# Optimization experiments

Measured on AMD Instinct MI355X. Metric: run time of the kernel, lower is better.

The kernel has to match this reference:

```python
import jax, jax.numpy as jnp
import numpy as np

B, S, T, D, H, FF = 2, 512, 64, 256, 8, 1024
DK = D // H
EPS = 1e-5


def setup_inputs() -> dict:
    key = jax.random.key(0)
    ks = jax.random.split(key, 24)
    sc = 1.0 / np.sqrt(D)
    inp = {"x": jax.random.normal(ks[0], (B, S, T, D), jnp.float32)}
    names = ["tq", "tk", "tv", "to", "sq", "sk", "sv", "so"]
    for i, n in enumerate(names):
        inp[n + "_w"] = jax.random.normal(ks[1 + 2 * i], (D, D), jnp.float32) * sc
        inp[n + "_b"] = jax.random.normal(ks[2 + 2 * i], (D,), jnp.float32) * sc
    inp["fc1_w"] = jax.random.normal(ks[17], (D, FF), jnp.float32) * sc
    inp["fc1_b"] = jnp.zeros((FF,), jnp.float32)
    inp["fc2_w"] = jax.random.normal(ks[18], (FF, D), jnp.float32) * (1.0 / np.sqrt(FF))
    inp["fc2_b"] = jnp.zeros((D,), jnp.float32)
    inp["ln1_w"] = jnp.ones((D,), jnp.float32)
    inp["ln1_b"] = jnp.zeros((D,), jnp.float32)
    inp["ln2_w"] = jnp.ones((D,), jnp.float32)
    inp["ln2_b"] = jnp.zeros((D,), jnp.float32)
    return inp


def _heads(x, w, b):
    # (B,S,T,D) -> (B,H,S,T,DK)
    Bx, Sx, Tx, Dx = x.shape
    return (x @ w + b).reshape(Bx, Sx, Tx, H, Dx // H).transpose(0, 3, 1, 2, 4)


def _merge(o, w, b):
    # (B,H,S,T,DK) -> (B,S,T,D)
    Bx, Hx, Sx, Tx, dk = o.shape
    return o.transpose(0, 2, 3, 1, 4).reshape(Bx, Sx, Tx, Hx * dk) @ w + b


def _ln(x, g, b):
    m = jnp.mean(x, -1, keepdims=True)
    v = jnp.mean((x - m) ** 2, -1, keepdims=True)
    return (x - m) * jax.lax.rsqrt(v + EPS) * g + b


def _forward(x, tq_w, tq_b, tk_w, tk_b, tv_w, tv_b, to_w, to_b,
             sq_w, sq_b, sk_w, sk_b, sv_w, sv_b, so_w, so_b,
             fc1_w, fc1_b, fc2_w, fc2_b, ln1_w, ln1_b, ln2_w, ln2_b):
    scale = 1.0 / np.sqrt(DK)
    # --- time attention (over T, independent per space point s) ---
    q = _heads(x, tq_w, tq_b)
    k = _heads(x, tk_w, tk_b)
    v = _heads(x, tv_w, tv_b)
    p = jax.nn.softmax(jnp.einsum('bhstd,bhsud->bhstu', q, k) * scale, axis=-1)
    tt = _merge(jnp.einsum('bhstu,bhsud->bhstd', p, v), to_w, to_b)
    # --- space attention (over S, independent per time step t) ---
    q = _heads(tt, sq_w, sq_b)
    k = _heads(tt, sk_w, sk_b)
    v = _heads(tt, sv_w, sv_b)
    p = jax.nn.softmax(jnp.einsum('bhstd,bhutd->bhtsu', q, k) * scale, axis=-1)
    so = _merge(jnp.einsum('bhtsu,bhutd->bhstd', p, v), so_w, so_b)
    # --- residual + post-LN, then FFN + residual + post-LN ---
    h = _ln(x + so, ln1_w, ln1_b)
    ff = jax.nn.relu(h @ fc1_w + fc1_b) @ fc2_w + fc2_b
    return _ln(h + ff, ln2_w, ln2_b)


def reference(x, tq_w, tq_b, tk_w, tk_b, tv_w, tv_b, to_w, to_b,
              sq_w, sq_b, sk_w, sk_b, sv_w, sv_b, so_w, so_b,
              fc1_w, fc1_b, fc2_w, fc2_b, ln1_w, ln1_b, ln2_w, ln2_b):
    return _forward(x, tq_w, tq_b, tk_w, tk_b, tv_w, tv_b, to_w, to_b,
                    sq_w, sq_b, sk_w, sk_b, sv_w, sv_b, so_w, so_b,
                    fc1_w, fc1_b, fc2_w, fc2_b, ln1_w, ln1_b, ln2_w, ln2_b)
```

## Files before the change

### kernel.cpp

```cpp
#include <hip/hip_runtime.h>
#include <hip/hip_bf16.h>

#define BB   2
#define SS   512
#define TT_  64
#define DD   256
#define HH   8
#define DKK  32
#define FFF  1024
#define NTOK 65536
#define EPSV 1e-5f
#define SCALE 0.17677669529663687f
#define S2F   0.25503486f
#define KPS  40
#define KP   40
#define VH   136
#define VP6  80

typedef unsigned short u16;
typedef unsigned int   u32;
typedef __attribute__((ext_vector_type(8))) short bf16x8;
typedef __attribute__((ext_vector_type(4))) short bf16x4;
typedef __attribute__((ext_vector_type(4))) float f32x4;

#if __has_builtin(__builtin_amdgcn_exp2f)
#define EXP2(x) __builtin_amdgcn_exp2f(x)
#else
#define EXP2(x) exp2f(x)
#endif

__device__ __forceinline__ float bf2f(u32 u) {
    union { u32 i; float f; } c; c.i = u << 16; return c.f;
}
__device__ __forceinline__ u16 f2bf(float f) {
    __hip_bfloat16 h = __float2bfloat16(f);
    return *reinterpret_cast<u16*>(&h);
}
__device__ __forceinline__ u32 cvtpk2(float lo, float hi) {
    float2 f; f.x = lo; f.y = hi;
    __hip_bfloat162 h2 = __float22bfloat162_rn(f);
    union { __hip_bfloat162 h; u32 u; } c; c.h = h2;
    return c.u;
}
__device__ __forceinline__ void load8v(const float* p, float* v) {
    *(float4*)(v)     = *(const float4*)(p);
    *(float4*)(v + 4) = *(const float4*)(p + 4);
}
__device__ __forceinline__ void load8v(const u16* p, float* v) {
    uint4 raw = *(const uint4*)(p);
    v[0] = bf2f(raw.x & 0xffffu); v[1] = bf2f(raw.x >> 16);
    v[2] = bf2f(raw.y & 0xffffu); v[3] = bf2f(raw.y >> 16);
    v[4] = bf2f(raw.z & 0xffffu); v[5] = bf2f(raw.z >> 16);
    v[6] = bf2f(raw.w & 0xffffu); v[7] = bf2f(raw.w >> 16);
}
__device__ __forceinline__ void load4v(const float* p, float* v) {
    float4 t = *(const float4*)p; v[0] = t.x; v[1] = t.y; v[2] = t.z; v[3] = t.w;
}
__device__ __forceinline__ void load4v(const u16* p, float* v) {
    uint2 raw = *(const uint2*)p;
    v[0] = bf2f(raw.x & 0xffffu); v[1] = bf2f(raw.x >> 16);
    v[2] = bf2f(raw.y & 0xffffu); v[3] = bf2f(raw.y >> 16);
}
__device__ __forceinline__ uint4 pack8bf(const float* v) {
    uint4 r;
    r.x = cvtpk2(v[0], v[1]); r.y = cvtpk2(v[2], v[3]);
    r.z = cvtpk2(v[4], v[5]); r.w = cvtpk2(v[6], v[7]);
    return r;
}
__device__ __forceinline__ uint2 pack4bf(const float* v) {
    uint2 r;
    r.x = cvtpk2(v[0], v[1]); r.y = cvtpk2(v[2], v[3]);
    return r;
}
__device__ __forceinline__ bf16x4 packbf4(const float* v) {
    union { uint2 u; bf16x4 h; } c;
    c.u = pack4bf(v);
    return c.h;
}
__device__ __forceinline__ void store4o(float* p, const float* v) {
    float4 t; t.x = v[0]; t.y = v[1]; t.z = v[2]; t.w = v[3];
    *(float4*)p = t;
}
__device__ __forceinline__ void store4o(u16* p, const float* v) {
    *(uint2*)p = pack4bf(v);
}
__device__ __forceinline__ void gl16(const u16* gsrc, u16* ldst) {
    __builtin_amdgcn_global_load_lds(
        (const __attribute__((address_space(1))) void*)gsrc,
        (__attribute__((address_space(3))) void*)ldst, 16, 0, 0);
}

#if __has_builtin(__builtin_amdgcn_mfma_f32_16x16x16bf16_1k)
__device__ __forceinline__ f32x4 mfma16(bf16x4 a, bf16x4 b, f32x4 c) {
    return __builtin_amdgcn_mfma_f32_16x16x16bf16_1k(a, b, c, 0, 0, 0);
}
#else
__device__ __forceinline__ f32x4 mfma16(bf16x4 a, bf16x4 b, f32x4 c) {
    asm("v_mfma_f32_16x16x16_bf16 %0, %1, %2, %0" : "+v"(c) : "v"(a), "v"(b));
    return c;
}
#endif

#define BF16_ONE ((short)0x3F80)

__global__ __launch_bounds__(256)
void transpose_w(const float* __restrict__ W, u16* __restrict__ WT, int K, int M,
                 float scale)
{
    __shared__ float t[32][33];
    const int mb = blockIdx.x * 32;
    const int kb = blockIdx.y * 32;
    const int lx = threadIdx.x & 31;
    const int ly = threadIdx.x >> 5;
    #pragma unroll
    for (int i = ly; i < 32; i += 8) t[i][lx] = W[(size_t)(kb + i) * M + mb + lx];
    __syncthreads();
    #pragma unroll
    for (int i = ly; i < 32; i += 8) WT[(size_t)(mb + i) * K + kb + lx] = f2bf(t[lx][i] * scale);
}

__global__ __launch_bounds__(256)
void pack_bias3(const float* __restrict__ a, const float* __restrict__ b,
                const float* __restrict__ c, float* __restrict__ out, float s0)
{
    const int i = threadIdx.x;
    out[i] = a[i] * s0; out[256 + i] = b[i]; out[512 + i] = c[i];
}

__global__ __launch_bounds__(256)
void fuse_to_sqkv_w(const float* __restrict__ to_w,
                    const float* __restrict__ sq_w, const float* __restrict__ sk_w,
                    const float* __restrict__ sv_w, u16* __restrict__ wt_out)
{
    const int m = blockIdx.x;
    const int k = threadIdx.x;
    const float* Wsq = (m < 256) ? sq_w : (m < 512 ? sk_w : sv_w);
    const int mc = m & 255;
    float acc = 0.f;
    for (int j = 0; j < 256; j++)
        acc += to_w[k * 256 + j] * Wsq[j * 256 + mc];
    if (m < 256) acc *= S2F;
    wt_out[m * 256 + k] = f2bf(acc);
}
__global__ __launch_bounds__(256)
void fuse_to_sqkv_b(const float* __restrict__ to_b,
                    const float* __restrict__ sq_w, const float* __restrict__ sk_w,
                    const float* __restrict__ sv_w,
                    const float* __restrict__ sq_b, const float* __restrict__ sk_b,
                    const float* __restrict__ sv_b, float* __restrict__ b_out)
{
    const int m = blockIdx.x * 256 + threadIdx.x;
    const float* Wsq = (blockIdx.x == 0) ? sq_w : (blockIdx.x == 1 ? sk_w : sv_w);
    const float* bs  = (blockIdx.x == 0) ? sq_b : (blockIdx.x == 1 ? sk_b : sv_b);
    const int mc = m & 255;
    float acc = bs[mc];
    for (int j = 0; j < 256; j++) acc += to_b[j] * Wsq[j * 256 + mc];
    if (blockIdx.x == 0) acc *= S2F;
    b_out[m] = acc;
}

__global__ __launch_bounds__(256)
void cvt_bf16(const float* __restrict__ in, u16* __restrict__ out, int n8)
{
    for (int i = blockIdx.x * blockDim.x + threadIdx.x; i < n8; i += gridDim.x * blockDim.x) {
        float v[8];
        load8v(in + (size_t)i * 8, v);
        *(uint4*)(out + (size_t)i * 8) = pack8bf(v);
    }
}

__global__ __launch_bounds__(512)
void gemm_bt6(const u16* __restrict__ A, int lda,
              const u16* __restrict__ WT,
              const float* __restrict__ bias, u16* __restrict__ C,
              int K, int M, int relu)
{
    __shared__ u16 As0[256 * 32];
    __shared__ u16 As1[256 * 32];
    __shared__ u16 Bs0[128 * 32];
    __shared__ u16 Bs1[128 * 32];
    const int tid  = threadIdx.x;
    const int wid  = tid >> 6;
    const int lane = tid & 63;
    const int l16  = lane & 15;
    const int kg   = lane >> 4;

    const int nwg = gridDim.x * gridDim.y;
    int lin = blockIdx.y * gridDim.x + blockIdx.x;
    lin = (lin & 7) * (nwg >> 3) + (lin >> 3);
    const int row0 = (lin / gridDim.x) * 256;
    const int col0 = (lin % gridDim.x) * 128;

    const int srow = lane >> 2;
    const int gchunk = ((lane & 3) ^ ((srow >> 1) & 3)) * 8;
    const int rchunk = (kg ^ ((l16 >> 1) & 3)) * 8;

    const u16* Abase = A  + (size_t)(row0 + srow) * lda + gchunk;
    const u16* Bbase = WT + (size_t)(col0 + wid * 16 + srow) * K + gchunk;

    f32x4 acc[2][8];
    #pragma unroll
    for (int fr = 0; fr < 2; fr++)
        #pragma unroll
        for (int fc = 0; fc < 8; fc++)
            acc[fr][fc] = (f32x4){0.f, 0.f, 0.f, 0.f};

#define STAGE_T(ASB, BSB, k0)                                                   \
    do {                                                                        \
        _Pragma("unroll")                                                       \
        for (int q = 0; q < 2; q++) {                                           \
            const int rbase = wid * 32 + q * 16;                                \
            gl16(Abase + (size_t)rbase * lda + (k0), &ASB[rbase * 32]);         \
        }                                                                       \
        gl16(Bbase + (k0), &BSB[wid * 16 * 32]);                                \
    } while (0)

#define COMPUTE_T(ASB, BSB)                                                     \
    do {                                                                        \
        bf16x8 af[2], bfr[8];                                                   \
        _Pragma("unroll")                                                       \
        for (int fr = 0; fr < 2; fr++)                                          \
            af[fr] = *(const bf16x8*)(&ASB[(wid * 32 + fr * 16 + l16) * 32 + rchunk]); \
        _Pragma("unroll")                                                       \
        for (int fc = 0; fc < 8; fc++)                                          \
            bfr[fc] = *(const bf16x8*)(&BSB[(fc * 16 + l16) * 32 + rchunk]);    \
        _Pragma("unroll")                                                       \
        for (int fr = 0; fr < 2; fr++)                                          \
            _Pragma("unroll")                                                   \
            for (int fc = 0; fc < 8; fc++)                                      \
                acc[fr][fc] = __builtin_amdgcn_mfma_f32_16x16x32_bf16(af[fr], bfr[fc], acc[fr][fc], 0, 0, 0); \
    } while (0)

    STAGE_T(As0, Bs0, 0);
    __syncthreads();

    for (int k0 = 0; k0 < K; k0 += 64) {
        if (k0 + 32 < K) STAGE_T(As1, Bs1, k0 + 32);
        COMPUTE_T(As0, Bs0);
        __syncthreads();
        if (k0 + 64 < K) STAGE_T(As0, Bs0, k0 + 64);
        COMPUTE_T(As1, Bs1);
        __syncthreads();
    }
#undef STAGE_T
#undef COMPUTE_T

    #pragma unroll
    for (int fr = 0; fr < 2; fr++) {
        #pragma unroll
        for (int fc = 0; fc < 8; fc++) {
            const int col = col0 + fc * 16 + l16;
            const float bv = bias[col];
            const int row = row0 + wid * 32 + fr * 16 + kg * 4;
            #pragma unroll
            for (int j = 0; j < 4; j += 2) {
                float x0 = acc[fr][fc][j]     + bv;
                float x1 = acc[fr][fc][j + 1] + bv;
                if (relu) { x0 = fmaxf(x0, 0.f); x1 = fmaxf(x1, 0.f); }
                const u32 pk = cvtpk2(x0, x1);
                C[(size_t)(row + j)     * M + col] = (u16)pk;
                C[(size_t)(row + j + 1) * M + col] = (u16)(pk >> 16);
            }
        }
    }
}

__global__ __launch_bounds__(512)
void gemm_bt6h(const u16* __restrict__ A, int lda,
               const u16* __restrict__ WT,
               const float* __restrict__ bias, u16* __restrict__ C,
               int K, int M, int relu)
{
    __shared__ u16 As0[128 * 32];
    __shared__ u16 As1[128 * 32];
    __shared__ u16 Bs0[128 * 32];
    __shared__ u16 Bs1[128 * 32];
    const int tid  = threadIdx.x;
    const int wid  = tid >> 6;
    const int lane = tid & 63;
    const int l16  = lane & 15;
    const int kg   = lane >> 4;

    const int nwg = gridDim.x * gridDim.y;
    int lin = blockIdx.y * gridDim.x + blockIdx.x;
    lin = (lin & 7) * (nwg >> 3) + (lin >> 3);
    const int row0 = (lin / gridDim.x) * 128;
    const int col0 = (lin % gridDim.x) * 128;

    const int srow = lane >> 2;
    const int gchunk = ((lane & 3) ^ ((srow >> 1) & 3)) * 8;
    const int rchunk = (kg ^ ((l16 >> 1) & 3)) * 8;

    const u16* Abase = A  + (size_t)(row0 + wid * 16 + srow) * lda + gchunk;
    const u16* Bbase = WT + (size_t)(col0 + wid * 16 + srow) * K + gchunk;

    f32x4 acc[8];
    #pragma unroll
    for (int fc = 0; fc < 8; fc++)
        acc[fc] = (f32x4){0.f, 0.f, 0.f, 0.f};

#define STAGE_H(ASB, BSB, k0)                                                   \
    do {                                                                        \
        gl16(Abase + (k0), &ASB[wid * 16 * 32]);                                \
        gl16(Bbase + (k0), &BSB[wid * 16 * 32]);                                \
    } while (0)

#define COMPUTE_H(ASB, BSB)                                                     \
    do {                                                                        \
        bf16x8 af, bfr[8];                                                      \
        af = *(const bf16x8*)(&ASB[(wid * 16 + l16) * 32 + rchunk]);            \
        _Pragma("unroll")                                                       \
        for (int fc = 0; fc < 8; fc++)                                          \
            bfr[fc] = *(const bf16x8*)(&BSB[(fc * 16 + l16) * 32 + rchunk]);    \
        _Pragma("unroll")                                                       \
        for (int fc = 0; fc < 8; fc++)                                          \
            acc[fc] = __builtin_amdgcn_mfma_f32_16x16x32_bf16(af, bfr[fc], acc[fc], 0, 0, 0); \
    } while (0)

    STAGE_H(As0, Bs0, 0);
    __syncthreads();

    for (int k0 = 0; k0 < K; k0 += 64) {
        if (k0 + 32 < K) STAGE_H(As1, Bs1, k0 + 32);
        COMPUTE_H(As0, Bs0);
        __syncthreads();
        if (k0 + 64 < K) STAGE_H(As0, Bs0, k0 + 64);
        COMPUTE_H(As1, Bs1);
        __syncthreads();
    }
#undef STAGE_H
#undef COMPUTE_H

    #pragma unroll
    for (int fc = 0; fc < 8; fc++) {
        const int col = col0 + fc * 16 + l16;
        const float bv = bias[col];
        const int row = row0 + wid * 16 + kg * 4;
        #pragma unroll
        for (int j = 0; j < 4; j += 2) {
            float x0 = acc[fc][j]     + bv;
            float x1 = acc[fc][j + 1] + bv;
            if (relu) { x0 = fmaxf(x0, 0.f); x1 = fmaxf(x1, 0.f); }
            const u32 pk = cvtpk2(x0, x1);
            C[(size_t)(row + j)     * M + col] = (u16)pk;
            C[(size_t)(row + j + 1) * M + col] = (u16)(pk >> 16);
        }
    }
}

__global__ __launch_bounds__(256)
void time_attn12(const u16* __restrict__ F, int ld, u16* __restrict__ O)
{
    __shared__ u16 Ks2[2][64 * KP];
    __shared__ u16 Vt2[2][32 * VP6];
    const int bid = blockIdx.x;
    const int tid  = threadIdx.x;
    const int wid  = tid >> 6;
    const int lane = tid & 63;
    const int l16  = lane & 15;
    const int g    = lane >> 4;

    #pragma unroll
    for (int it = 0; it < 2; it++) {
        const int i = tid + it * 256;
        const int tu = i >> 8, rr = (i >> 2) & 63, p = i & 3;
        const int tau = bid * 2 + tu;
        const size_t ga = ((size_t)(tau >> 3) * 64 + rr) * ld + (tau & 7) * DKK + 256 + p * 8;
        *(uint4*)&Ks2[tu][rr * KP + p * 8] = *(const uint4*)(F + ga);
    }
    #pragma unroll
    for (int it = 0; it < 2; it++) {
        const int i = tid + it * 256;
        const int tu = i >> 8, p = (i >> 6) & 3, rr = i & 63;
        const int tau = bid * 2 + tu;
        const size_t ga = ((size_t)(tau >> 3) * 64 + rr) * ld + (tau & 7) * DKK + 512 + p * 8;
        uint4 vv = *(const uint4*)(F + ga);
        const u16* vp = (const u16*)&vv;
        #pragma unroll
        for (int j = 0; j < 8; j++) Vt2[tu][(p * 8 + j) * VP6 + rr] = vp[j];
    }
    __syncthreads();

    const int tu  = wid >> 1;
    const int tau = bid * 2 + tu;
    const int hc  = (tau & 7) * DKK;
    const size_t n0 = (size_t)(tau >> 3) * 64;
    const int q0  = (wid & 1) * 32;
    const f32x4 z4 = (f32x4){0.f, 0.f, 0.f, 0.f};
    const bf16x4 vone = (bf16x4){BF16_ONE, BF16_ONE, BF16_ONE, BF16_ONE};

    bf16x8 qf[2];
    #pragma unroll
    for (int f = 0; f < 2; f++)
        qf[f] = *(const bf16x8*)(F + (n0 + q0 + f * 16 + l16) * ld + hc + g * 8);

    f32x4 s[2][4];
    #pragma unroll
    for (int kt = 0; kt < 4; kt++) {
        bf16x8 kf = *(const bf16x8*)&Ks2[tu][(kt * 16 + l16) * KP + g * 8];
        s[0][kt] = __builtin_amdgcn_mfma_f32_16x16x32_bf16(kf, qf[0], z4, 0, 0, 0);
        s[1][kt] = __builtin_amdgcn_mfma_f32_16x16x32_bf16(kf, qf[1], z4, 0, 0, 0);
    }

    bf16x4 pp[2][4];
    #pragma unroll
    for (int f = 0; f < 2; f++) {
        #pragma unroll
        for (int kt = 0; kt < 4; kt++) {
            float pv[4];
            #pragma unroll
            for (int j = 0; j < 4; j++) pv[j] = EXP2(s[f][kt][j]);
            pp[f][kt] = packbf4(pv);
        }
    }

    f32x4 o[2][2];
    f32x4 lacc[2];
    #pragma unroll
    for (int f = 0; f < 2; f++) {
        lacc[f] = z4;
        #pragma unroll
        for (int hh = 0; hh < 2; hh++)
            o[f][hh] = z4;
    }
    #pragma unroll
    for (int kt = 0; kt < 4; kt++) {
        bf16x4 vf[2];
        #pragma unroll
        for (int hh = 0; hh < 2; hh++)
            vf[hh] = *(const bf16x4*)&Vt2[tu][(hh * 16 + l16) * VP6 + kt * 16 + g * 4];
        #pragma unroll
        for (int f = 0; f < 2; f++) {
            o[f][0] = mfma16(pp[f][kt], vf[0], o[f][0]);
            o[f][1] = mfma16(pp[f][kt], vf[1], o[f][1]);
            lacc[f] = mfma16(pp[f][kt], vone, lacc[f]);
        }
    }

    #pragma unroll
    for (int f = 0; f < 2; f++) {
        float iv[4];
        #pragma unroll
        for (int j = 0; j < 4; j++) iv[j] = 1.f / lacc[f][j];
        #pragma unroll
        for (int hh = 0; hh < 2; hh++) {
            const u32 p0 = cvtpk2(o[f][hh][0] * iv[0], o[f][hh][1] * iv[1]);
            const u32 p1 = cvtpk2(o[f][hh][2] * iv[2], o[f][hh][3] * iv[3]);
            const size_t ga0 = (n0 + q0 + f * 16 + g * 4) * DD + hc + hh * 16 + l16;
            O[ga0]          = (u16)p0;
            O[ga0 + DD]     = (u16)(p0 >> 16);
            O[ga0 + 2 * DD] = (u16)p1;
            O[ga0 + 3 * DD] = (u16)(p1 >> 16);
        }
    }
}

__global__ __launch_bounds__(512, 4)
void space_attn16(u16* __restrict__ F, int ld)
{
    __shared__ u16 Ks[2][128 * KPS];
    __shared__ u16 Vt[2][32 * VH];
    const int bid = blockIdx.x;
    const int t  = bid & (TT_ - 1);
    const int h  = (bid >> 6) & (HH - 1);
    const int b  = bid >> 9;
    const int hc = h * DKK;
    const int tid  = threadIdx.x;
    const int wid  = tid >> 6;
    const int lane = tid & 63;
    const int l16  = lane & 15;
    const int g    = lane >> 4;

    const int kr = tid >> 2, kp = tid & 3;
    const int vr = tid & 127, vp = tid >> 7;
    const size_t rowstr = (size_t)TT_ * ld;
    const size_t base0  = ((size_t)(b * SS) * TT_ + t) * ld + hc;

    const int q0 = wid * 64;
    bf16x8 qf[4];
    #pragma unroll
    for (int f = 0; f < 4; f++) {
        const int s = q0 + f * 16 + l16;
        qf[f] = *(const bf16x8*)(F + base0 + (size_t)s * rowstr + g * 8);
    }

    uint4 kreg = *(const uint4*)(F + base0 + 256 + (size_t)kr * rowstr + kp * 8);
    uint4 vreg = *(const uint4*)(F + base0 + 512 + (size_t)vr * rowstr + vp * 8);
    *(uint4*)&Ks[0][kr * KPS + kp * 8] = kreg;
    {
        const u16* vpp = (const u16*)&vreg;
        #pragma unroll
        for (int j = 0; j < 8; j++) Vt[0][(vp * 8 + j) * VH + vr] = vpp[j];
    }
    __syncthreads();

    f32x4 o[4][2];
    f32x4 lacc[4];
    const f32x4 z4 = (f32x4){0.f, 0.f, 0.f, 0.f};
    const bf16x4 vone = (bf16x4){BF16_ONE, BF16_ONE, BF16_ONE, BF16_ONE};
    #pragma unroll
    for (int f = 0; f < 4; f++) {
        lacc[f] = z4;
        #pragma unroll
        for (int hh = 0; hh < 2; hh++)
            o[f][hh] = z4;
    }

    for (int qtr = 0; qtr < 4; qtr++) {
        const int cur = qtr & 1;
        if (qtr < 3) {
            const int key = (qtr + 1) * 128;
            kreg = *(const uint4*)(F + base0 + 256 + (size_t)(key + kr) * rowstr + kp * 8);
            vreg = *(const uint4*)(F + base0 + 512 + (size_t)(key + vr) * rowstr + vp * 8);
        }

        for (int kc2 = 0; kc2 < 4; kc2++) {
            bf16x8 kfa = *(const bf16x8*)&Ks[cur][(kc2 * 32 +      l16) * KPS + g * 8];
            bf16x8 kfb = *(const bf16x8*)&Ks[cur][(kc2 * 32 + 16 + l16) * KPS + g * 8];

            bf16x4 pa[4], pb[4];
            #pragma unroll
            for (int f = 0; f < 4; f++) {
                f32x4 sa = __builtin_amdgcn_mfma_f32_16x16x32_bf16(kfa, qf[f], z4, 0, 0, 0);
                f32x4 sb = __builtin_amdgcn_mfma_f32_16x16x32_bf16(kfb, qf[f], z4, 0, 0, 0);
                float pva[4], pvb[4];
                #pragma unroll
                for (int j = 0; j < 4; j++) pva[j] = EXP2(sa[j]);
                #pragma unroll
                for (int j = 0; j < 4; j++) pvb[j] = EXP2(sb[j]);
                pa[f] = packbf4(pva);
                pb[f] = packbf4(pvb);
            }

            bf16x4 va[2][2];
            #pragma unroll
            for (int hh = 0; hh < 2; hh++)
                #pragma unroll
                for (int u = 0; u < 2; u++)
                    va[hh][u] = *(const bf16x4*)&Vt[cur][(hh * 16 + l16) * VH + kc2 * 32 + u * 16 + g * 4];

            __builtin_amdgcn_s_setprio(1);
            #pragma unroll
            for (int f = 0; f < 4; f++) {
                #pragma unroll
                for (int hh = 0; hh < 2; hh++) {
                    o[f][hh] = mfma16(pa[f], va[hh][0], o[f][hh]);
                    o[f][hh] = mfma16(pb[f], va[hh][1], o[f][hh]);
                }
                lacc[f] = mfma16(pa[f], vone, lacc[f]);
                lacc[f] = mfma16(pb[f], vone, lacc[f]);
            }
            __builtin_amdgcn_s_setprio(0);
        }

        if (qtr < 3) {
            __syncthreads();
            *(uint4*)&Ks[cur ^ 1][kr * KPS + kp * 8] = kreg;
            const u16* vpp = (const u16*)&vreg;
            #pragma unroll
            for (int j = 0; j < 8; j++) Vt[cur ^ 1][(vp * 8 + j) * VH + vr] = vpp[j];
            __syncthreads();
        }
    }

    #pragma unroll
    for (int f = 0; f < 4; f++) {
        float iv[4];
        #pragma unroll
        for (int j = 0; j < 4; j++) iv[j] = 1.f / lacc[f][j];
        const int s = q0 + f * 16 + g * 4;
        #pragma unroll
        for (int hh = 0; hh < 2; hh++) {
            const u32 p0 = cvtpk2(o[f][hh][0] * iv[0], o[f][hh][1] * iv[1]);
            const u32 p1 = cvtpk2(o[f][hh][2] * iv[2], o[f][hh][3] * iv[3]);
            const size_t ga0 = base0 + (size_t)s * rowstr + hh * 16 + l16;
            F[ga0]              = (u16)p0;
            F[ga0 + rowstr]     = (u16)(p0 >> 16);
            F[ga0 + 2 * rowstr] = (u16)p1;
            F[ga0 + 3 * rowstr] = (u16)(p1 >> 16);
        }
    }
}

template<typename T1, typename TO>
__global__ __launch_bounds__(256)
void add_ln(const T1* __restrict__ X1, const u16* __restrict__ X2,
            const float* __restrict__ gw, const float* __restrict__ bw,
            TO* __restrict__ out)
{
    const int row  = blockIdx.x * 4 + (threadIdx.x >> 6);
    const int lane = threadIdx.x & 63;
    const size_t base = (size_t)row * DD + lane * 4;
    float v[4], w2[4];
    load4v(X1 + base, v);
    load4v(X2 + base, w2);
    v[0] += w2[0]; v[1] += w2[1]; v[2] += w2[2]; v[3] += w2[3];
    float s1 = v[0] + v[1] + v[2] + v[3];
    float s2 = v[0]*v[0] + v[1]*v[1] + v[2]*v[2] + v[3]*v[3];
    #pragma unroll
    for (int o = 1; o < 64; o <<= 1) { s1 += __shfl_xor(s1, o); s2 += __shfl_xor(s2, o); }
    const float mean = s1 * (1.f / DD);
    const float var  = s2 * (1.f / DD) - mean * mean;
    const float rs   = rsqrtf(var + EPSV);
    float o4[4];
    #pragma unroll
    for (int i = 0; i < 4; i++) {
        const int d = lane * 4 + i;
        o4[i] = (v[i] - mean) * rs * gw[d] + bw[d];
    }
    store4o(out + base, o4);
}

extern "C" void kernel_launch(void* const* d_in, const int* in_sizes, int n_in,
                              void* d_out, int out_size, void* d_ws, size_t ws_size,
                              hipStream_t stream)
{
    (void)in_sizes; (void)n_in; (void)out_size;
    const float* x     = (const float*)d_in[0];
    const float* tq_w  = (const float*)d_in[1];
    const float* tq_b  = (const float*)d_in[2];
    const float* tk_w  = (const float*)d_in[3];
    const float* tk_b  = (const float*)d_in[4];
    const float* tv_w  = (const float*)d_in[5];
    const float* tv_b  = (const float*)d_in[6];
    const float* to_w  = (const float*)d_in[7];
    const float* to_b  = (const float*)d_in[8];
    const float* sq_w  = (const float*)d_in[9];
    const float* sq_b  = (const float*)d_in[10];
    const float* sk_w  = (const float*)d_in[11];
    const float* sk_b  = (const float*)d_in[12];
    const float* sv_w  = (const float*)d_in[13];
    const float* sv_b  = (const float*)d_in[14];
    const float* so_w  = (const float*)d_in[15];
    const float* so_b  = (const float*)d_in[16];
    const float* fc1_w = (const float*)d_in[17];
    const float* fc1_b = (const float*)d_in[18];
    const float* fc2_w = (const float*)d_in[19];
    const float* fc2_b = (const float*)d_in[20];
    const float* ln1_w = (const float*)d_in[21];
    const float* ln1_b = (const float*)d_in[22];
    const float* ln2_w = (const float*)d_in[23];
    const float* ln2_b = (const float*)d_in[24];

    const size_t SLOT = (size_t)NTOK * DD;
    u16*   F  = (u16*)d_ws;
    u16*   W0 = (u16*)d_ws;
    u16*   W1 = W0 + SLOT;
    u16*   OA = (u16*)d_out;
    float* HD = (float*)d_out;
    u16*   WTb = (u16*)((char*)d_out + (61u << 20));
    float* BIb = (float*)((char*)d_out + (63u << 20));

    const bool ffn1 = ws_size >= 6 * SLOT * sizeof(u16);
    u16* W2 = ffn1 ? (W1 + 4 * SLOT) : (W1 + SLOT);

    u16* wt_tqkv  = WTb;
    u16* wt_fused = wt_tqkv + 3 * 65536;
    u16* wt_so    = wt_fused + 3 * 65536;
    u16* wt_fc1   = wt_so + 65536;
    u16* wt_fc2   = wt_fc1 + 262144;
    float* b_tqkv  = BIb;
    float* b_fused = BIb + 768;

    dim3 blk(256);
    dim3 blk5(512);
    dim3 gT(DD / 32, DD / 32);

    transpose_w<<<gT, blk, 0, stream>>>(tq_w, wt_tqkv,              DD, DD, S2F);
    transpose_w<<<gT, blk, 0, stream>>>(tk_w, wt_tqkv + 65536,      DD, DD, 1.0f);
    transpose_w<<<gT, blk, 0, stream>>>(tv_w, wt_tqkv + 2 * 65536,  DD, DD, 1.0f);
    transpose_w<<<gT, blk, 0, stream>>>(so_w, wt_so, DD, DD, 1.0f);
    transpose_w<<<dim3(FFF / 32, DD / 32), blk, 0, stream>>>(fc1_w, wt_fc1, DD, FFF, 1.0f);
    transpose_w<<<dim3(DD / 32, FFF / 32), blk, 0, stream>>>(fc2_w, wt_fc2, FFF, DD, 1.0f);
    pack_bias3<<<1, blk, 0, stream>>>(tq_b, tk_b, tv_b, b_tqkv, S2F);
    fuse_to_sqkv_w<<<768, blk, 0, stream>>>(to_w, sq_w, sk_w, sv_w, wt_fused);
    fuse_to_sqkv_b<<<3, blk, 0, stream>>>(to_b, sq_w, sk_w, sv_w, sq_b, sk_b, sv_b, b_fused);

    cvt_bf16<<<2048, blk, 0, stream>>>(x, OA, (int)(SLOT / 8));

    dim3 gqkv(768 / 128, NTOK / 256);
    dim3 gd(DD / 128, NTOK / 256);

    gemm_bt6<<<gqkv, blk5, 0, stream>>>(OA, DD, wt_tqkv, b_tqkv, F, DD, 768, 0);
    time_attn12<<<BB * HH * SS / 2, blk, 0, stream>>>(F, 768, OA);

    gemm_bt6<<<gqkv, blk5, 0, stream>>>(OA, DD, wt_fused, b_fused, F, DD, 768, 0);
    space_attn16<<<BB * HH * TT_, blk5, 0, stream>>>(F, 768);
    gemm_bt6<<<gd, blk5, 0, stream>>>(F, 768, wt_so, so_b, OA, DD, DD, 0);

    add_ln<float, u16><<<NTOK / 4, blk, 0, stream>>>(x, OA, ln1_w, ln1_b, W0);

    if (ffn1) {
        gemm_bt6<<<dim3(FFF / 128, NTOK / 256), blk5, 0, stream>>>(W0, DD, wt_fc1, fc1_b, W1, DD, FFF, 1);
        gemm_bt6h<<<dim3(DD / 128, NTOK / 128), blk5, 0, stream>>>(W1, FFF, wt_fc2, fc2_b, W2, FFF, DD, 0);
        add_ln<u16, float><<<NTOK / 4, blk, 0, stream>>>(W0, W2, ln2_w, ln2_b, HD);
    } else {
        for (int c = 0; c < 4; c++) {
            const size_t off = (size_t)c * 16384 * DD;
            gemm_bt6<<<dim3(FFF / 128, 16384 / 256), blk5, 0, stream>>>(W0 + off, DD, wt_fc1, fc1_b, W1, DD, FFF, 1);
            gemm_bt6h<<<dim3(DD / 128, 16384 / 128), blk5, 0, stream>>>(W1, FFF, wt_fc2, fc2_b, W2, FFF, DD, 0);
            add_ln<u16, float><<<16384 / 4, blk, 0, stream>>>(W0 + off, W2, ln2_w, ln2_b, HD + off);
        }
    }
}
```

Baseline: 420.0 us.

## Fuse LayerNorm epilogues into full-row output GEMMs for so-proj and fc2

Adds a gemm_ln kernel in which each workgroup computes a 128x256 tile covering the full D width. Bias, residual add and LayerNorm run in the epilogue using in-wave shuffles. This replaces the so-projection GEMM plus add_ln and the fc2 GEMM plus add_ln, which removes two intermediate activation round trips through memory and two launches. The trade-offs are fewer workgroups (512) with 16 accumulator tiles per wave, so register pressure rises and occupancy may drop. Workspace layout also changes: weights move into the workspace when it is large enough.

Result: faster. 406.3 us (-3.3%).

```diff
diff --git a/kernel.cpp b/kernel.cpp
--- a/kernel.cpp
+++ b/kernel.cpp
@@ -84,6 +84,10 @@
 __device__ __forceinline__ void store4o(u16* p, const float* v) {
     *(uint2*)p = pack4bf(v);
 }
+__device__ __forceinline__ float rload(const float* p) { return *p; }
+__device__ __forceinline__ float rload(const u16* p)  { return bf2f(*p); }
+__device__ __forceinline__ void sstore(float* p, float v) { *p = v; }
+__device__ __forceinline__ void sstore(u16* p, float v)   { *p = f2bf(v); }
 __device__ __forceinline__ void gl16(const u16* gsrc, u16* ldst) {
     __builtin_amdgcn_global_load_lds(
         (const __attribute__((address_space(1))) void*)gsrc,
@@ -345,6 +349,106 @@
             C[(size_t)(row + j)     * M + col] = (u16)pk;
             C[(size_t)(row + j + 1) * M + col] = (u16)(pk >> 16);
         }
+    }
+}
+
+template<typename TR, typename TO>
+__global__ __launch_bounds__(512)
+void gemm_ln(const u16* __restrict__ A, int lda,
+             const u16* __restrict__ WT,
+             const float* __restrict__ bias,
+             const TR* __restrict__ R,
+             const float* __restrict__ gw, const float* __restrict__ bw,
+             TO* __restrict__ out, int K)
+{
+    __shared__ u16 As0[128 * 32];
+    __shared__ u16 As1[128 * 32];
+    __shared__ u16 Bs0[256 * 32];
+    __shared__ u16 Bs1[256 * 32];
+    const int tid  = threadIdx.x;
+    const int wid  = tid >> 6;
+    const int lane = tid & 63;
+    const int l16  = lane & 15;
+    const int kg   = lane >> 4;
+
+    const int nwg = gridDim.x;
+    int lin = blockIdx.x;
+    lin = (lin & 7) * (nwg >> 3) + (lin >> 3);
+    const int row0 = lin * 128;
+
+    const int srow = lane >> 2;
+    const int gchunk = ((lane & 3) ^ ((srow >> 1) & 3)) * 8;
+    const int rchunk = (kg ^ ((l16 >> 1) & 3)) * 8;
+
+    const u16* Abase = A  + (size_t)(row0 + wid * 16 + srow) * lda + gchunk;
+    const u16* Bbase = WT + (size_t)(wid * 32 + srow) * K + gchunk;
+
+    f32x4 acc[16];
+    #pragma unroll
+    for (int fc = 0; fc < 16; fc++)
+        acc[fc] = (f32x4){0.f, 0.f, 0.f, 0.f};
+
+#define STAGE_L(ASB, BSB, k0)                                                   \
+    do {                                                                        \
+        gl16(Abase + (k0), &ASB[wid * 16 * 32]);                                \
+        _Pragma("unroll")                                                       \
+        for (int q = 0; q < 2; q++) {                                           \
+            const int rbase = wid * 32 + q * 16;                                \
+            gl16(Bbase + (size_t)(q * 16) * K + (k0), &BSB[rbase * 32]);        \
+        }                                                                       \
+    } while (0)
+
+#define COMPUTE_L(ASB, BSB)                                                     \
+    do {                                                                        \
+        bf16x8 af, bfr[16];                                                     \
+        af = *(const bf16x8*)(&ASB[(wid * 16 + l16) * 32 + rchunk]);            \
+        _Pragma("unroll")                                                       \
+        for (int fc = 0; fc < 16; fc++)                                         \
+            bfr[fc] = *(const bf16x8*)(&BSB[(fc * 16 + l16) * 32 + rchunk]);    \
+        _Pragma("unroll")                                                       \
+        for (int fc = 0; fc < 16; fc++)                                         \
+            acc[fc] = __builtin_amdgcn_mfma_f32_16x16x32_bf16(af, bfr[fc], acc[fc], 0, 0, 0); \
+    } while (0)
+
+    STAGE_L(As0, Bs0, 0);
+    __syncthreads();
+
+    for (int k0 = 0; k0 < K; k0 += 64) {
+        if (k0 + 32 < K) STAGE_L(As1, Bs1, k0 + 32);
+        COMPUTE_L(As0, Bs0);
+        __syncthreads();
+        if (k0 + 64 < K) STAGE_L(As0, Bs0, k0 + 64);
+        COMPUTE_L(As1, Bs1);
+        __syncthreads();
+    }
+#undef STAGE_L
+#undef COMPUTE_L
+
+    float bia[16], gwv[16], bwv[16];
+    #pragma unroll
+    for (int fc = 0; fc < 16; fc++) {
+        const int d = fc * 16 + l16;
+        bia[fc] = bias[d]; gwv[fc] = gw[d]; bwv[fc] = bw[d];
+    }
+    #pragma unroll
+    for (int j = 0; j < 4; j++) {
+        const int row = row0 + wid * 16 + kg * 4 + j;
+        const size_t rb = (size_t)row * DD + l16;
+        float v[16];
+        float s1 = 0.f, s2 = 0.f;
+        #pragma unroll
+        for (int fc = 0; fc < 16; fc++) {
+            const float xv = acc[fc][j] + bia[fc] + rload(R + rb + fc * 16);
+            v[fc] = xv; s1 += xv; s2 += xv * xv;
+        }
+        #pragma unroll
+        for (int o = 1; o < 16; o <<= 1) { s1 += __shfl_xor(s1, o); s2 += __shfl_xor(s2, o); }
+        const float mean = s1 * (1.f / DD);
+        const float var  = s2 * (1.f / DD) - mean * mean;
+        const float rs   = rsqrtf(var + EPSV);
+        #pragma unroll
+        for (int fc = 0; fc < 16; fc++)
+            sstore(out + rb + fc * 16, (v[fc] - mean) * rs * gwv[fc] + bwv[fc]);
     }
 }
 
@@ -644,15 +748,14 @@
 
     const size_t SLOT = (size_t)NTOK * DD;
     u16*   F  = (u16*)d_ws;
-    u16*   W0 = (u16*)d_ws;
-    u16*   W1 = W0 + SLOT;
     u16*   OA = (u16*)d_out;
     float* HD = (float*)d_out;
-    u16*   WTb = (u16*)((char*)d_out + (61u << 20));
-    float* BIb = (float*)((char*)d_out + (63u << 20));
 
     const bool ffn1 = ws_size >= 6 * SLOT * sizeof(u16);
-    u16* W2 = ffn1 ? (W1 + 4 * SLOT) : (W1 + SLOT);
+    u16*   WTb = ffn1 ? ((u16*)d_ws + 4 * SLOT)
+                      : (u16*)((char*)d_out + (61u << 20));
+    float* BIb = ffn1 ? (float*)((u16*)d_ws + 4 * SLOT + 983040)
+                      : (float*)((char*)d_out + (63u << 20));
 
     u16* wt_tqkv  = WTb;
     u16* wt_fused = wt_tqkv + 3 * 65536;
@@ -679,22 +782,29 @@
     cvt_bf16<<<2048, blk, 0, stream>>>(x, OA, (int)(SLOT / 8));
 
     dim3 gqkv(768 / 128, NTOK / 256);
-    dim3 gd(DD / 128, NTOK / 256);
 
     gemm_bt6<<<gqkv, blk5, 0, stream>>>(OA, DD, wt_tqkv, b_tqkv, F, DD, 768, 0);
     time_attn12<<<BB * HH * SS / 2, blk, 0, stream>>>(F, 768, OA);
 
     gemm_bt6<<<gqkv, blk5, 0, stream>>>(OA, DD, wt_fused, b_fused, F, DD, 768, 0);
     space_attn16<<<BB * HH * TT_, blk5, 0, stream>>>(F, 768);
-    gemm_bt6<<<gd, blk5, 0, stream>>>(F, 768, wt_so, so_b, OA, DD, DD, 0);
-
-    add_ln<float, u16><<<NTOK / 4, blk, 0, stream>>>(x, OA, ln1_w, ln1_b, W0);
 
     if (ffn1) {
-        gemm_bt6<<<dim3(FFF / 128, NTOK / 256), blk5, 0, stream>>>(W0, DD, wt_fc1, fc1_b, W1, DD, FFF, 1);
-        gemm_bt6h<<<dim3(DD / 128, NTOK / 128), blk5, 0, stream>>>(W1, FFF, wt_fc2, fc2_b, W2, FFF, DD, 0);
-        add_ln<u16, float><<<NTOK / 4, blk, 0, stream>>>(W0, W2, ln2_w, ln2_b, HD);
+        u16* HB   = (u16*)d_ws + 5 * SLOT;
+        u16* W1FF = (u16*)d_ws;
+        gemm_ln<float, u16><<<NTOK / 128, blk5, 0, stream>>>(
+            F, 768, wt_so, so_b, x, ln1_w, ln1_b, HB, DD);
+        gemm_bt6<<<dim3(FFF / 128, NTOK / 256), blk5, 0, stream>>>(
+            HB, DD, wt_fc1, fc1_b, W1FF, DD, FFF, 1);
+        gemm_ln<u16, float><<<NTOK / 128, blk5, 0, stream>>>(
+            W1FF, FFF, wt_fc2, fc2_b, HB, ln2_w, ln2_b, HD, FFF);
     } else {
+        u16* W0 = (u16*)d_ws;
+        u16* W1 = W0 + SLOT;
+        u16* W2 = W1 + SLOT;
+        dim3 gd(DD / 128, NTOK / 256);
+        gemm_bt6<<<gd, blk5, 0, stream>>>(F, 768, wt_so, so_b, OA, DD, DD, 0);
+        add_ln<float, u16><<<NTOK / 4, blk, 0, stream>>>(x, OA, ln1_w, ln1_b, W0);
         for (int c = 0; c < 4; c++) {
             const size_t off = (size_t)c * 16384 * DD;
             gemm_bt6<<<dim3(FFF / 128, 16384 / 256), blk5, 0, stream>>>(W0 + off, DD, wt_fc1, fc1_b, W1, DD, FFF, 1);
```
